# Optimization experiments

Measured on AMD Instinct MI355X. Metric: run time of the kernel, lower is better.

## Reference

```python
import jax, jax.numpy as jnp
import numpy as np

B, S, H, P = 16, 8192, 512, 32

def setup_inputs() -> dict:
    key = jax.random.key(0)
    k1, k2 = jax.random.split(key)
    birnn_outputs = jax.random.normal(k1, (B, S, H), dtype=jnp.float32)
    self_attn = jax.random.normal(k2, (P, H), dtype=jnp.float32)
    return {"birnn_outputs": birnn_outputs, "self_attn": self_attn}

def reference(birnn_outputs, self_attn):
    # scores: [B, P, S] = probes [P,H] x birnn_outputs^T [B,H,S]
    scores = jnp.einsum('ph,bsh->bps', self_attn, birnn_outputs)
    attn = jax.nn.softmax(scores, axis=-1)  # softmax over seq_len
    # context: [B, P, H]
    ctx = jnp.einsum('bps,bsh->bph', attn, birnn_outputs)
    return ctx.reshape(ctx.shape[0], -1)  # [B, P*H]
```

## Files before the change

### kernel.cpp

```cpp
#include <hip/hip_runtime.h>
#include <hip/hip_bf16.h>

#define BB 16
#define SS 8192
#define HH 512
#define PP 32

typedef __attribute__((ext_vector_type(8))) short short8;
typedef __attribute__((ext_vector_type(4))) float f32x4;
typedef __attribute__((ext_vector_type(2))) unsigned int u32x2;

__device__ inline unsigned short bf16_hi_trunc(float x) {
  union { float f; unsigned u; } v; v.f = x;
  return (unsigned short)(v.u >> 16);
}
__device__ inline unsigned short bf16_rne(float x) {
  union { float f; unsigned u; } v; v.f = x;
  unsigned r = v.u + 0x7FFFu + ((v.u >> 16) & 1u);
  return (unsigned short)(r >> 16);
}
__device__ inline float from_hi(unsigned short h) {
  union { unsigned u; float f; } v; v.u = ((unsigned)h) << 16;
  return v.f;
}
__device__ inline f32x4 max4(f32x4 a, f32x4 b) {
  f32x4 r; r.x = fmaxf(a.x, b.x); r.y = fmaxf(a.y, b.y);
  r.z = fmaxf(a.z, b.z); r.w = fmaxf(a.w, b.w); return r;
}
__device__ inline f32x4 exp4(f32x4 a) {
  f32x4 r; r.x = __expf(a.x); r.y = __expf(a.y);
  r.z = __expf(a.z); r.w = __expf(a.w); return r;
}
__device__ inline f32x4 fma_b(float a, f32x4 b, f32x4 c) {
  c.x = fmaf(a, b.x, c.x); c.y = fmaf(a, b.y, c.y);
  c.z = fmaf(a, b.z, c.z); c.w = fmaf(a, b.w, c.w); return c;
}

__global__ void k_prep(const float* __restrict__ probes,
                       short* __restrict__ Ph, short* __restrict__ Pl) {
  int t = threadIdx.x;
  for (int q = t; q < 2048; q += 256) {
    int lane = q & 63, kcg = (q >> 6) & 15, nt = q >> 10;
    int p = nt * 16 + (lane & 15);
    int h0 = kcg * 32 + (lane >> 4) * 8;
#pragma unroll
    for (int j = 0; j < 8; ++j) {
      float f = probes[p * HH + h0 + j];
      unsigned short h = bf16_hi_trunc(f);
      Ph[q * 8 + j] = (short)h;
      Pl[q * 8 + j] = (short)bf16_rne(f - from_hi(h));
    }
  }
}

__global__ __launch_bounds__(256) void k_scores3(
    const float* __restrict__ x, const short* __restrict__ Ph,
    const short* __restrict__ Pl, float* __restrict__ scoresT) {
  __shared__ __align__(16) short Bh[64 * 128];
  __shared__ __align__(16) short Bl[64 * 128];
  const int t = threadIdx.x;
  const int lane = t & 63, w = t >> 6;
  const int b = blockIdx.y;
  const int stile = blockIdx.x;

  f32x4 acc[2];
  acc[0] = (f32x4){0.f, 0.f, 0.f, 0.f};
  acc[1] = (f32x4){0.f, 0.f, 0.f, 0.f};

  const int frow = w * 16 + (lane & 15);
  const int g4 = lane >> 4;

  for (int hc = 0; hc < 4; ++hc) {
    if (hc) __syncthreads();
#pragma unroll
    for (int it = 0; it < 8; ++it) {
      int g = t + 256 * it;
      int row = g >> 5, u = g & 31;
      f32x4 v = *(const f32x4*)(x + ((size_t)b * SS + stile * 64 + row) * HH +
                                hc * 128 + u * 4);
      unsigned short h0 = bf16_hi_trunc(v.x), h1 = bf16_hi_trunc(v.y);
      unsigned short h2 = bf16_hi_trunc(v.z), h3 = bf16_hi_trunc(v.w);
      u32x2 hi, lo;
      hi.x = (unsigned)h0 | ((unsigned)h1 << 16);
      hi.y = (unsigned)h2 | ((unsigned)h3 << 16);
      lo.x = (unsigned)bf16_rne(v.x - from_hi(h0)) |
             ((unsigned)bf16_rne(v.y - from_hi(h1)) << 16);
      lo.y = (unsigned)bf16_rne(v.z - from_hi(h2)) |
             ((unsigned)bf16_rne(v.w - from_hi(h3)) << 16);
      int qsw = ((u >> 1) ^ (row & 15));
      int idx = row * 128 + qsw * 8 + (u & 1) * 4;
      *(u32x2*)&Bh[idx] = hi;
      *(u32x2*)&Bl[idx] = lo;
    }
    __syncthreads();

#pragma unroll
    for (int kc = 0; kc < 4; ++kc) {
      int qr = ((kc * 4 + g4) ^ (frow & 15));
      short8 xh = *(const short8*)&Bh[frow * 128 + qr * 8];
      short8 xl = *(const short8*)&Bl[frow * 128 + qr * 8];
      int kcg = hc * 4 + kc;
#pragma unroll
      for (int nt = 0; nt < 2; ++nt) {
        short8 ph = *(const short8*)(Ph + ((size_t)((nt * 16 + kcg) * 64 + lane)) * 8);
        short8 pl = *(const short8*)(Pl + ((size_t)((nt * 16 + kcg) * 64 + lane)) * 8);
        acc[nt] = __builtin_amdgcn_mfma_f32_16x16x32_bf16(xh, ph, acc[nt], 0, 0, 0);
        acc[nt] = __builtin_amdgcn_mfma_f32_16x16x32_bf16(xh, pl, acc[nt], 0, 0, 0);
        acc[nt] = __builtin_amdgcn_mfma_f32_16x16x32_bf16(xl, ph, acc[nt], 0, 0, 0);
      }
    }
  }

#pragma unroll
  for (int nt = 0; nt < 2; ++nt)
#pragma unroll
    for (int r = 0; r < 4; ++r) {
      int s = stile * 64 + w * 16 + (lane >> 4) * 4 + r;
      int p = nt * 16 + (lane & 15);
      scoresT[((size_t)b * SS + s) * PP + p] = acc[nt][r];
    }
}

__global__ __launch_bounds__(256) void k_stats_a(
    const float* __restrict__ scoresT, float* __restrict__ pm,
    float* __restrict__ pl_) {
  const int blk = blockIdx.x;
  const int b = blk >> 3, sr = blk & 7;
  const int t = threadIdx.x;
  const int p4 = t & 7, sg = t >> 3;
  const f32x4* base = (const f32x4*)(scoresT + ((size_t)b * SS + sr * 1024) * PP);

  f32x4 m4 = (f32x4){-1e30f, -1e30f, -1e30f, -1e30f};
  f32x4 l4 = (f32x4){0.f, 0.f, 0.f, 0.f};
#pragma unroll 4
  for (int i = 0; i < 32; ++i) {
    int s = sg + 32 * i;
    f32x4 v = base[s * 8 + p4];
    f32x4 nm = max4(m4, v);
    l4 = l4 * exp4(m4 - nm) + exp4(v - nm);
    m4 = nm;
  }
  __shared__ f32x4 sm[32][8], sl[32][8];
  sm[sg][p4] = m4;
  sl[sg][p4] = l4;
  __syncthreads();
  if (t < 8) {
    f32x4 M = sm[0][t], L = sl[0][t];
#pragma unroll 4
    for (int i = 1; i < 32; ++i) {
      f32x4 m2 = sm[i][t], l2 = sl[i][t];
      f32x4 nm = max4(M, m2);
      L = L * exp4(M - nm) + l2 * exp4(m2 - nm);
      M = nm;
    }
    *(f32x4*)&pm[blk * PP + t * 4] = M;
    *(f32x4*)&pl_[blk * PP + t * 4] = L;
  }
}

__global__ __launch_bounds__(256) void k_stats_b(
    const float* __restrict__ pm, const float* __restrict__ pl_,
    float* __restrict__ Mv, float* __restrict__ invl) {
  int i = blockIdx.x * 256 + threadIdx.x;
  if (i >= BB * PP) return;
  int b = i >> 5, p = i & 31;
  float M = -1e30f, L = 0.f;
#pragma unroll
  for (int sr = 0; sr < 8; ++sr) {
    float m2 = pm[(b * 8 + sr) * PP + p], l2 = pl_[(b * 8 + sr) * PP + p];
    float nm = fmaxf(M, m2);
    L = L * __expf(M - nm) + l2 * __expf(m2 - nm);
    M = nm;
  }
  Mv[i] = M;
  invl[i] = 1.0f / L;
}

__global__ __launch_bounds__(256) void k_ctx3(
    const float* __restrict__ x, const float* __restrict__ scoresT,
    const float* __restrict__ Mv, const float* __restrict__ invl,
    float* __restrict__ part) {
  __shared__ float wl[512 * PP];
  const int t = threadIdx.x;
  const int lane = t & 63, w = t >> 6;
  const int sc = blockIdx.x, hh = blockIdx.y, b = blockIdx.z;

  const int pbase = (4 * t) & 31;
  f32x4 mv = *(const f32x4*)(Mv + b * PP + pbase);
  f32x4 il = *(const f32x4*)(invl + b * PP + pbase);
  const f32x4* src = (const f32x4*)(scoresT + ((size_t)b * SS + sc * 512) * PP);
#pragma unroll
  for (int it = 0; it < 16; ++it) {
    f32x4 v = src[t + 256 * it];
    f32x4 e;
    e.x = __expf(v.x - mv.x) * il.x;
    e.y = __expf(v.y - mv.y) * il.y;
    e.z = __expf(v.z - mv.z) * il.z;
    e.w = __expf(v.w - mv.w) * il.w;
    *(f32x4*)&wl[(t + 256 * it) * 4] = e;
  }
  __syncthreads();

  const float* xrow = x + ((size_t)b * SS + sc * 512) * HH + hh * 256 + lane * 4;
  const f32x4* wj = (const f32x4*)wl;

  f32x4 acc[8];
#pragma unroll
  for (int k = 0; k < 8; ++k) acc[k] = (f32x4){0.f, 0.f, 0.f, 0.f};

#pragma unroll 4
  for (int j = 0; j < 512; ++j) {
    f32x4 xv = *(const f32x4*)(xrow + (size_t)j * HH);
    f32x4 w0 = wj[j * 8 + w * 2];
    f32x4 w1 = wj[j * 8 + w * 2 + 1];
    acc[0] = fma_b(w0.x, xv, acc[0]);
    acc[1] = fma_b(w0.y, xv, acc[1]);
    acc[2] = fma_b(w0.z, xv, acc[2]);
    acc[3] = fma_b(w0.w, xv, acc[3]);
    acc[4] = fma_b(w1.x, xv, acc[4]);
    acc[5] = fma_b(w1.y, xv, acc[5]);
    acc[6] = fma_b(w1.z, xv, acc[6]);
    acc[7] = fma_b(w1.w, xv, acc[7]);
  }

#pragma unroll
  for (int pi = 0; pi < 8; ++pi) {
    int p = w * 8 + pi;
    *(f32x4*)(part + (((size_t)sc * BB + b) * PP + p) * HH + hh * 256 + lane * 4) =
        acc[pi];
  }
}

__global__ __launch_bounds__(256) void k_reduce(const float* __restrict__ part,
                                               float* __restrict__ out) {
  int i = blockIdx.x * 256 + threadIdx.x;
  float s = 0.f;
#pragma unroll
  for (int c = 0; c < 16; ++c) s += part[(size_t)c * (BB * PP * HH) + i];
  out[i] = s;
}

extern "C" void kernel_launch(void* const* d_in, const int* in_sizes, int n_in,
                              void* d_out, int out_size, void* d_ws, size_t ws_size,
                              hipStream_t stream) {
  const float* x = (const float*)d_in[0];
  const float* probes = (const float*)d_in[1];
  float* out = (float*)d_out;

  float* scoresT = (float*)d_ws;
  float* part = scoresT + (size_t)BB * SS * PP;
  float* Mv = part + (size_t)16 * BB * PP * HH;
  float* invl = Mv + BB * PP;
  float* pm = invl + BB * PP;
  float* pl_ = pm + 128 * PP;
  short* Ph = (short*)(pl_ + 128 * PP);
  short* Pl = Ph + PP * HH;

  k_prep<<<1, 256, 0, stream>>>(probes, Ph, Pl);
  k_scores3<<<dim3(SS / 64, BB), 256, 0, stream>>>(x, Ph, Pl, scoresT);
  k_stats_a<<<dim3(128), 256, 0, stream>>>(scoresT, pm, pl_);
  k_stats_b<<<dim3(2), 256, 0, stream>>>(pm, pl_, Mv, invl);
  k_ctx3<<<dim3(16, 2, BB), 256, 0, stream>>>(x, scoresT, Mv, invl, part);
  k_reduce<<<dim3(BB * PP * HH / 256), 256, 0, stream>>>(part, out);
}
```

Measured before the change: 484.0 us.

## Load score operands directly to registers and double seq-chunk parallelism for stats and context

The scores kernel drops its shared-memory staging and barriers: each lane loads its MFMA fragment of x straight from global memory and splits it into hi/lo bf16 in registers. The stats and context kernels split the sequence into 32 chunks of 256 instead of 16 or 8 chunks, giving more blocks to fill the GPU. The context loop batches eight row loads ahead of the FMAs to expose more memory-level parallelism. In exchange, the partial-sum buffer and final reduction double in size, and the direct global loads in the scores kernel are strided per lane rather than coalesced.

New measurement: 472.1 us. 1.03x faster.

```diff
diff --git a/kernel.cpp b/kernel.cpp
--- a/kernel.cpp
+++ b/kernel.cpp
@@ -8,7 +8,6 @@
 
 typedef __attribute__((ext_vector_type(8))) short short8;
 typedef __attribute__((ext_vector_type(4))) float f32x4;
-typedef __attribute__((ext_vector_type(2))) unsigned int u32x2;
 
 __device__ inline unsigned short bf16_hi_trunc(float x) {
   union { float f; unsigned u; } v; v.f = x;
@@ -34,6 +33,14 @@
 __device__ inline f32x4 fma_b(float a, f32x4 b, f32x4 c) {
   c.x = fmaf(a, b.x, c.x); c.y = fmaf(a, b.y, c.y);
   c.z = fmaf(a, b.z, c.z); c.w = fmaf(a, b.w, c.w); return c;
+}
+__device__ inline void cvt8(const float* xv, short8& bh, short8& bl) {
+#pragma unroll
+  for (int j = 0; j < 8; ++j) {
+    unsigned short h = bf16_hi_trunc(xv[j]);
+    bh[j] = (short)h;
+    bl[j] = (short)bf16_rne(xv[j] - from_hi(h));
+  }
 }
 
 __global__ void k_prep(const float* __restrict__ probes,
@@ -53,11 +60,9 @@
   }
 }
 
-__global__ __launch_bounds__(256) void k_scores3(
+__global__ __launch_bounds__(256) void k_scores4(
     const float* __restrict__ x, const short* __restrict__ Ph,
     const short* __restrict__ Pl, float* __restrict__ scoresT) {
-  __shared__ __align__(16) short Bh[64 * 128];
-  __shared__ __align__(16) short Bl[64 * 128];
   const int t = threadIdx.x;
   const int lane = t & 63, w = t >> 6;
   const int b = blockIdx.y;
@@ -67,48 +72,26 @@
   acc[0] = (f32x4){0.f, 0.f, 0.f, 0.f};
   acc[1] = (f32x4){0.f, 0.f, 0.f, 0.f};
 
-  const int frow = w * 16 + (lane & 15);
-  const int g4 = lane >> 4;
-
-  for (int hc = 0; hc < 4; ++hc) {
-    if (hc) __syncthreads();
-#pragma unroll
-    for (int it = 0; it < 8; ++it) {
-      int g = t + 256 * it;
-      int row = g >> 5, u = g & 31;
-      f32x4 v = *(const f32x4*)(x + ((size_t)b * SS + stile * 64 + row) * HH +
-                                hc * 128 + u * 4);
-      unsigned short h0 = bf16_hi_trunc(v.x), h1 = bf16_hi_trunc(v.y);
-      unsigned short h2 = bf16_hi_trunc(v.z), h3 = bf16_hi_trunc(v.w);
-      u32x2 hi, lo;
-      hi.x = (unsigned)h0 | ((unsigned)h1 << 16);
-      hi.y = (unsigned)h2 | ((unsigned)h3 << 16);
-      lo.x = (unsigned)bf16_rne(v.x - from_hi(h0)) |
-             ((unsigned)bf16_rne(v.y - from_hi(h1)) << 16);
-      lo.y = (unsigned)bf16_rne(v.z - from_hi(h2)) |
-             ((unsigned)bf16_rne(v.w - from_hi(h3)) << 16);
-      int qsw = ((u >> 1) ^ (row & 15));
-      int idx = row * 128 + qsw * 8 + (u & 1) * 4;
-      *(u32x2*)&Bh[idx] = hi;
-      *(u32x2*)&Bl[idx] = lo;
-    }
-    __syncthreads();
-
-#pragma unroll
-    for (int kc = 0; kc < 4; ++kc) {
-      int qr = ((kc * 4 + g4) ^ (frow & 15));
-      short8 xh = *(const short8*)&Bh[frow * 128 + qr * 8];
-      short8 xl = *(const short8*)&Bl[frow * 128 + qr * 8];
-      int kcg = hc * 4 + kc;
-#pragma unroll
-      for (int nt = 0; nt < 2; ++nt) {
-        short8 ph = *(const short8*)(Ph + ((size_t)((nt * 16 + kcg) * 64 + lane)) * 8);
-        short8 pl = *(const short8*)(Pl + ((size_t)((nt * 16 + kcg) * 64 + lane)) * 8);
-        acc[nt] = __builtin_amdgcn_mfma_f32_16x16x32_bf16(xh, ph, acc[nt], 0, 0, 0);
-        acc[nt] = __builtin_amdgcn_mfma_f32_16x16x32_bf16(xh, pl, acc[nt], 0, 0, 0);
-        acc[nt] = __builtin_amdgcn_mfma_f32_16x16x32_bf16(xl, ph, acc[nt], 0, 0, 0);
-      }
-    }
+  const int srow = stile * 64 + w * 16 + (lane & 15);
+  const float* xr = x + ((size_t)b * SS + srow) * HH + (lane >> 4) * 8;
+
+#pragma unroll 2
+  for (int kcg = 0; kcg < 16; ++kcg) {
+    f32x4 xa = *(const f32x4*)(xr + kcg * 32);
+    f32x4 xc = *(const f32x4*)(xr + kcg * 32 + 4);
+    float xv[8] = {xa.x, xa.y, xa.z, xa.w, xc.x, xc.y, xc.z, xc.w};
+    short8 xh, xl;
+    cvt8(xv, xh, xl);
+    short8 ph0 = *(const short8*)(Ph + ((size_t)(kcg * 64 + lane)) * 8);
+    short8 pl0 = *(const short8*)(Pl + ((size_t)(kcg * 64 + lane)) * 8);
+    short8 ph1 = *(const short8*)(Ph + ((size_t)((16 + kcg) * 64 + lane)) * 8);
+    short8 pl1 = *(const short8*)(Pl + ((size_t)((16 + kcg) * 64 + lane)) * 8);
+    acc[0] = __builtin_amdgcn_mfma_f32_16x16x32_bf16(xh, ph0, acc[0], 0, 0, 0);
+    acc[0] = __builtin_amdgcn_mfma_f32_16x16x32_bf16(xh, pl0, acc[0], 0, 0, 0);
+    acc[0] = __builtin_amdgcn_mfma_f32_16x16x32_bf16(xl, ph0, acc[0], 0, 0, 0);
+    acc[1] = __builtin_amdgcn_mfma_f32_16x16x32_bf16(xh, ph1, acc[1], 0, 0, 0);
+    acc[1] = __builtin_amdgcn_mfma_f32_16x16x32_bf16(xh, pl1, acc[1], 0, 0, 0);
+    acc[1] = __builtin_amdgcn_mfma_f32_16x16x32_bf16(xl, ph1, acc[1], 0, 0, 0);
   }
 
 #pragma unroll
@@ -125,15 +108,15 @@
     const float* __restrict__ scoresT, float* __restrict__ pm,
     float* __restrict__ pl_) {
   const int blk = blockIdx.x;
-  const int b = blk >> 3, sr = blk & 7;
+  const int b = blk >> 5, sr = blk & 31;
   const int t = threadIdx.x;
   const int p4 = t & 7, sg = t >> 3;
-  const f32x4* base = (const f32x4*)(scoresT + ((size_t)b * SS + sr * 1024) * PP);
+  const f32x4* base = (const f32x4*)(scoresT + ((size_t)b * SS + sr * 256) * PP);
 
   f32x4 m4 = (f32x4){-1e30f, -1e30f, -1e30f, -1e30f};
   f32x4 l4 = (f32x4){0.f, 0.f, 0.f, 0.f};
-#pragma unroll 4
-  for (int i = 0; i < 32; ++i) {
+#pragma unroll
+  for (int i = 0; i < 8; ++i) {
     int s = sg + 32 * i;
     f32x4 v = base[s * 8 + p4];
     f32x4 nm = max4(m4, v);
@@ -146,7 +129,7 @@
   __syncthreads();
   if (t < 8) {
     f32x4 M = sm[0][t], L = sl[0][t];
-#pragma unroll 4
+#pragma unroll
     for (int i = 1; i < 32; ++i) {
       f32x4 m2 = sm[i][t], l2 = sl[i][t];
       f32x4 nm = max4(M, m2);
@@ -166,8 +149,8 @@
   int b = i >> 5, p = i & 31;
   float M = -1e30f, L = 0.f;
 #pragma unroll
-  for (int sr = 0; sr < 8; ++sr) {
-    float m2 = pm[(b * 8 + sr) * PP + p], l2 = pl_[(b * 8 + sr) * PP + p];
+  for (int sr = 0; sr < 32; ++sr) {
+    float m2 = pm[(b * 32 + sr) * PP + p], l2 = pl_[(b * 32 + sr) * PP + p];
     float nm = fmaxf(M, m2);
     L = L * __expf(M - nm) + l2 * __expf(m2 - nm);
     M = nm;
@@ -176,11 +159,11 @@
   invl[i] = 1.0f / L;
 }
 
-__global__ __launch_bounds__(256) void k_ctx3(
+__global__ __launch_bounds__(256) void k_ctx4(
     const float* __restrict__ x, const float* __restrict__ scoresT,
     const float* __restrict__ Mv, const float* __restrict__ invl,
     float* __restrict__ part) {
-  __shared__ float wl[512 * PP];
+  __shared__ float wl[256 * PP];
   const int t = threadIdx.x;
   const int lane = t & 63, w = t >> 6;
   const int sc = blockIdx.x, hh = blockIdx.y, b = blockIdx.z;
@@ -188,9 +171,9 @@
   const int pbase = (4 * t) & 31;
   f32x4 mv = *(const f32x4*)(Mv + b * PP + pbase);
   f32x4 il = *(const f32x4*)(invl + b * PP + pbase);
-  const f32x4* src = (const f32x4*)(scoresT + ((size_t)b * SS + sc * 512) * PP);
-#pragma unroll
-  for (int it = 0; it < 16; ++it) {
+  const f32x4* src = (const f32x4*)(scoresT + ((size_t)b * SS + sc * 256) * PP);
+#pragma unroll
+  for (int it = 0; it < 8; ++it) {
     f32x4 v = src[t + 256 * it];
     f32x4 e;
     e.x = __expf(v.x - mv.x) * il.x;
@@ -201,26 +184,32 @@
   }
   __syncthreads();
 
-  const float* xrow = x + ((size_t)b * SS + sc * 512) * HH + hh * 256 + lane * 4;
+  const float* xrow = x + ((size_t)b * SS + sc * 256) * HH + hh * 256 + lane * 4;
   const f32x4* wj = (const f32x4*)wl;
 
   f32x4 acc[8];
 #pragma unroll
   for (int k = 0; k < 8; ++k) acc[k] = (f32x4){0.f, 0.f, 0.f, 0.f};
 
-#pragma unroll 4
-  for (int j = 0; j < 512; ++j) {
-    f32x4 xv = *(const f32x4*)(xrow + (size_t)j * HH);
-    f32x4 w0 = wj[j * 8 + w * 2];
-    f32x4 w1 = wj[j * 8 + w * 2 + 1];
-    acc[0] = fma_b(w0.x, xv, acc[0]);
-    acc[1] = fma_b(w0.y, xv, acc[1]);
-    acc[2] = fma_b(w0.z, xv, acc[2]);
-    acc[3] = fma_b(w0.w, xv, acc[3]);
-    acc[4] = fma_b(w1.x, xv, acc[4]);
-    acc[5] = fma_b(w1.y, xv, acc[5]);
-    acc[6] = fma_b(w1.z, xv, acc[6]);
-    acc[7] = fma_b(w1.w, xv, acc[7]);
+  for (int jo = 0; jo < 256; jo += 8) {
+    f32x4 xv[8];
+#pragma unroll
+    for (int u = 0; u < 8; ++u)
+      xv[u] = *(const f32x4*)(xrow + (size_t)(jo + u) * HH);
+#pragma unroll
+    for (int u = 0; u < 8; ++u) {
+      int j = jo + u;
+      f32x4 w0 = wj[j * 8 + w * 2];
+      f32x4 w1 = wj[j * 8 + w * 2 + 1];
+      acc[0] = fma_b(w0.x, xv[u], acc[0]);
+      acc[1] = fma_b(w0.y, xv[u], acc[1]);
+      acc[2] = fma_b(w0.z, xv[u], acc[2]);
+      acc[3] = fma_b(w0.w, xv[u], acc[3]);
+      acc[4] = fma_b(w1.x, xv[u], acc[4]);
+      acc[5] = fma_b(w1.y, xv[u], acc[5]);
+      acc[6] = fma_b(w1.z, xv[u], acc[6]);
+      acc[7] = fma_b(w1.w, xv[u], acc[7]);
+    }
   }
 
 #pragma unroll
@@ -236,7 +225,7 @@
   int i = blockIdx.x * 256 + threadIdx.x;
   float s = 0.f;
 #pragma unroll
-  for (int c = 0; c < 16; ++c) s += part[(size_t)c * (BB * PP * HH) + i];
+  for (int c = 0; c < 32; ++c) s += part[(size_t)c * (BB * PP * HH) + i];
   out[i] = s;
 }
 
@@ -249,17 +238,17 @@
 
   float* scoresT = (float*)d_ws;
   float* part = scoresT + (size_t)BB * SS * PP;
-  float* Mv = part + (size_t)16 * BB * PP * HH;
+  float* Mv = part + (size_t)32 * BB * PP * HH;
   float* invl = Mv + BB * PP;
   float* pm = invl + BB * PP;
-  float* pl_ = pm + 128 * PP;
-  short* Ph = (short*)(pl_ + 128 * PP);
+  float* pl_ = pm + 512 * PP;
+  short* Ph = (short*)(pl_ + 512 * PP);
   short* Pl = Ph + PP * HH;
 
   k_prep<<<1, 256, 0, stream>>>(probes, Ph, Pl);
-  k_scores3<<<dim3(SS / 64, BB), 256, 0, stream>>>(x, Ph, Pl, scoresT);
-  k_stats_a<<<dim3(128), 256, 0, stream>>>(scoresT, pm, pl_);
+  k_scores4<<<dim3(SS / 64, BB), 256, 0, stream>>>(x, Ph, Pl, scoresT);
+  k_stats_a<<<dim3(512), 256, 0, stream>>>(scoresT, pm, pl_);
   k_stats_b<<<dim3(2), 256, 0, stream>>>(pm, pl_, Mv, invl);
-  k_ctx3<<<dim3(16, 2, BB), 256, 0, stream>>>(x, scoresT, Mv, invl, part);
+  k_ctx4<<<dim3(32, 2, BB), 256, 0, stream>>>(x, scoresT, Mv, invl, part);
   k_reduce<<<dim3(BB * PP * HH / 256), 256, 0, stream>>>(part, out);
 }
```
